# Kernel optimization log

Measured on AMD Instinct MI355X. Metric: run time of the kernel, lower is better.

Reference implementation:

```python
import jax, jax.numpy as jnp
import numpy as np

B, C_IN, H, W = 8, 32, 64, 64
C = 64  # num_channels


def setup_inputs() -> dict:
    key = jax.random.key(0)
    ks = jax.random.split(key, 9)
    s_in = 1.0 / np.sqrt(C_IN)
    s_c = 1.0 / np.sqrt(C)
    return {
        "x": jax.random.normal(ks[0], (B, C_IN, H, W), dtype=jnp.float32),
        "wq": jax.random.uniform(ks[1], (C, C_IN), jnp.float32, -s_in, s_in),
        "bq": jax.random.uniform(ks[2], (C,), jnp.float32, -s_in, s_in),
        "wk": jax.random.uniform(ks[3], (C, C_IN), jnp.float32, -s_in, s_in),
        "bk": jax.random.uniform(ks[4], (C,), jnp.float32, -s_in, s_in),
        "wv": jax.random.uniform(ks[5], (C, C_IN), jnp.float32, -s_in, s_in),
        "bv": jax.random.uniform(ks[6], (C,), jnp.float32, -s_in, s_in),
        "wo": jax.random.uniform(ks[7], (C_IN, C), jnp.float32, -s_c, s_c),
        "bo": jax.random.uniform(ks[8], (C_IN,), jnp.float32, -s_c, s_c),
    }


def reference(x, wq, bq, wk, bk, wv, bv, wo, bo):
    b, c_in, h, w = x.shape
    n = h * w
    # 1x1 convs == per-pixel linear projections; produce (B, N, C) directly
    q = (jnp.einsum('bchw,oc->bhwo', x, wq) + bq).reshape(b, n, -1)
    k = (jnp.einsum('bchw,oc->bhwo', x, wk) + bk).reshape(b, n, -1)
    v = (jnp.einsum('bchw,oc->bhwo', x, wv) + bv).reshape(b, n, -1)
    # unscaled attention over spatial positions (no 1/sqrt(d) in original)
    scores = jnp.einsum('bnc,bmc->bnm', q, k)  # (B, N, N)
    attn = jax.nn.softmax(scores, axis=-1)
    out = jnp.einsum('bnm,bmc->bnc', attn, v)  # (B, N, C)
    out = out.reshape(b, h, w, -1)
    out = jnp.einsum('bhwc,oc->bohw', out, wo) + bo[None, :, None, None]
    return out + x
```

## Files before the change

kernel.cpp:

```cpp
#include <hip/hip_runtime.h>
#include <hip/hip_bf16.h>

#define CIN    32
#define NPIX   4096
#define DIM    64
#define LOG2E  1.4426950408889634f

#if __has_builtin(__builtin_amdgcn_exp2f)
#define EXP2(x) __builtin_amdgcn_exp2f(x)
#else
#define EXP2(x) exp2f(x)
#endif

typedef float  f32x4  __attribute__((ext_vector_type(4)));
typedef float  f32x16 __attribute__((ext_vector_type(16)));
typedef short  s16x8  __attribute__((ext_vector_type(8)));

#define ZERO16 {0.f,0.f,0.f,0.f,0.f,0.f,0.f,0.f,0.f,0.f,0.f,0.f,0.f,0.f,0.f,0.f}

__device__ __forceinline__ f32x16 mfma32(s16x8 a, s16x8 b, f32x16 c) {
    return __builtin_amdgcn_mfma_f32_32x32x16_bf16(a, b, c, 0, 0, 0);
}


__global__ __launch_bounds__(256) void qkv_proj(
    const float* __restrict__ x,
    const float* __restrict__ wq, const float* __restrict__ bq,
    const float* __restrict__ wk, const float* __restrict__ bk,
    const float* __restrict__ wv, const float* __restrict__ bv,
    __hip_bfloat16* __restrict__ qb, __hip_bfloat16* __restrict__ kb,
    __hip_bfloat16* __restrict__ vb)
{
    const int tid  = threadIdx.x;
    const int wid  = tid >> 6;
    const int lane = tid & 63;
    const int l31  = lane & 31;
    const int hl   = lane >> 5;
    const int b    = blockIdx.y;
    const int bx   = blockIdx.x;
    const int s    = bx * 4 + wid;
    const int px   = s * 32 + l31;

    s16x8 xhi[2], xlo[2];
    #pragma unroll
    for (int kt = 0; kt < 2; kt++) {
        union { s16x8 v; __hip_bfloat16 h8[8]; } uh, ul;
        #pragma unroll
        for (int j = 0; j < 8; j++) {
            const int c = kt * 16 + hl * 8 + j;
            const float xv = x[((size_t)b * CIN + c) * NPIX + px];
            const __hip_bfloat16 hi = __float2bfloat16(xv);
            uh.h8[j] = hi;
            ul.h8[j] = __float2bfloat16(xv - __bfloat162float(hi));
        }
        xhi[kt] = uh.v; xlo[kt] = ul.v;
    }

    auto do_mat = [&](const float* __restrict__ W, const float* __restrict__ B,
                      int which) {
        const float scale = (which == 0) ? LOG2E : 1.0f;
        s16x8 whi[2][2], wlo[2][2];
        #pragma unroll
        for (int t = 0; t < 2; t++)
            #pragma unroll
            for (int kt = 0; kt < 2; kt++) {
                const float* wp = W + (size_t)(t * 32 + l31) * CIN + kt * 16 + hl * 8;
                f32x4 a0 = *(const f32x4*)wp;
                f32x4 a1 = *(const f32x4*)(wp + 4);
                union { s16x8 v; __hip_bfloat16 h8[8]; } uh, ul;
                #pragma unroll
                for (int j = 0; j < 4; j++) {
                    const float v0 = a0[j] * scale, v1 = a1[j] * scale;
                    const __hip_bfloat16 h0 = __float2bfloat16(v0);
                    const __hip_bfloat16 h1 = __float2bfloat16(v1);
                    uh.h8[j] = h0; uh.h8[4 + j] = h1;
                    ul.h8[j]     = __float2bfloat16(v0 - __bfloat162float(h0));
                    ul.h8[4 + j] = __float2bfloat16(v1 - __bfloat162float(h1));
                }
                whi[t][kt] = uh.v; wlo[t][kt] = ul.v;
            }

        f32x16 acc0 = ZERO16, acc1 = ZERO16;
        if (which < 2) {
            #pragma unroll
            for (int kt = 0; kt < 2; kt++) {
                acc0 = mfma32(whi[0][kt], xhi[kt], acc0);
                acc1 = mfma32(whi[1][kt], xhi[kt], acc1);
                acc0 = mfma32(whi[0][kt], xlo[kt], acc0);
                acc1 = mfma32(whi[1][kt], xlo[kt], acc1);
                acc0 = mfma32(wlo[0][kt], xhi[kt], acc0);
                acc1 = mfma32(wlo[1][kt], xhi[kt], acc1);
            }
            #pragma unroll
            for (int t = 0; t < 2; t++) {
                const f32x16 acc = t ? acc1 : acc0;
                #pragma unroll
                for (int ig = 0; ig < 4; ig++) {
                    f32x4 b4 = *(const f32x4*)(B + t * 32 + ig * 8 + hl * 4);
                    union { unsigned long long u; __hip_bfloat16 h4[4]; } st;
                    #pragma unroll
                    for (int r = 0; r < 4; r++)
                        st.h4[r] = __float2bfloat16(acc[ig * 4 + r] + b4[r] * scale);
                    if (which == 0) {
                        const size_t off = ((size_t)b * NPIX + px) * DIM
                                         + t * 32 + ig * 8 + hl * 4;
                        *(unsigned long long*)(qb + off) = st.u;
                    } else {
                        const size_t off = (size_t)b * 262144
                            + ((size_t)(s * 4 + 2 * t + (ig >> 1)) * 64
                               + (ig & 1) * 32 + l31) * 8 + 4 * hl;
                        *(unsigned long long*)(kb + off) = st.u;
                    }
                }
            }
        } else {
            #pragma unroll
            for (int kt = 0; kt < 2; kt++) {
                acc0 = mfma32(xhi[kt], whi[0][kt], acc0);
                acc1 = mfma32(xhi[kt], whi[1][kt], acc1);
                acc0 = mfma32(xlo[kt], whi[0][kt], acc0);
                acc1 = mfma32(xlo[kt], whi[1][kt], acc1);
                acc0 = mfma32(xhi[kt], wlo[0][kt], acc0);
                acc1 = mfma32(xhi[kt], wlo[1][kt], acc1);
            }
            #pragma unroll
            for (int t = 0; t < 2; t++) {
                const f32x16 acc = t ? acc1 : acc0;
                const float bvv = B[t * 32 + l31];
                #pragma unroll
                for (int m = 0; m < 2; m++) {
                    union { s16x8 v; __hip_bfloat16 h8[8]; } st;
                    #pragma unroll
                    for (int e = 0; e < 8; e++)
                        st.h8[e] = __float2bfloat16(acc[m * 8 + e] + bvv);
                    const size_t off = (size_t)b * 262144
                        + ((size_t)(s * 4 + 2 * t + m) * 64 + hl * 32 + l31) * 8;
                    *(s16x8*)(vb + off) = st.v;
                }
            }
        }
    };

    do_mat(wq, bq, 0);
    do_mat(wk, bk, 1);
    do_mat(wv, bv, 2);
}

__global__ __launch_bounds__(512, 2) void attn_fused(
    const __hip_bfloat16* __restrict__ qb,
    const __hip_bfloat16* __restrict__ kbf,
    const __hip_bfloat16* __restrict__ vbf,
    const float* __restrict__ wo, const float* __restrict__ bo,
    const float* __restrict__ x, float* __restrict__ y)
{
    __shared__ __align__(16) char  sm[2][8][4096];
    __shared__ __align__(16) float REDx[4][64][33];
    __shared__ float LRED2[4][32];

    const int tid  = threadIdx.x;
    const int w    = tid >> 6;
    const int g    = w >> 1;
    const int h    = w & 1;
    const int lane = tid & 63;
    const int q    = lane & 31;
    const int hl   = lane >> 5;
    const int b    = blockIdx.x;
    const int row0 = blockIdx.y * 128 + g * 32;

    s16x8 qf[4];
    #pragma unroll
    for (int kt = 0; kt < 4; kt++)
        qf[kt] = *(const s16x8*)(qb + ((size_t)b * NPIX + row0 + q) * DIM
                                 + kt * 16 + hl * 8);

    f32x16 o0 = ZERO16, o1 = ZERO16;
    float lsacc = 0.f;

    const char* stbase = ((w >> 2) ? (const char*)vbf : (const char*)kbf)
                       + (size_t)b * 524288
                       + (size_t)((w >> 1) & 1) * 262144
                       + (size_t)(w & 1) * 4096
                       + (size_t)lane * 16;
    char* std0 = &sm[0][w][lane * 16];
    char* std1 = &sm[1][w][lane * 16];

    #pragma unroll
    for (int i = 0; i < 4; i++)
        *(f32x4*)(std0 + i * 1024) = *(const f32x4*)(stbase + i * 1024);
    __syncthreads();

    int cur = 0;
    for (int p = 0; p < 32; ++p) {
        const size_t srcoff = (size_t)((p < 31) ? p + 1 : 31) * 8192;
        f32x4 r0 = *(const f32x4*)(stbase + srcoff);
        f32x4 r1 = *(const f32x4*)(stbase + srcoff + 1024);
        f32x4 r2 = *(const f32x4*)(stbase + srcoff + 2048);
        f32x4 r3 = *(const f32x4*)(stbase + srcoff + 3072);

        const char* K0 = sm[cur][h * 2 + 0];
        const char* K1 = sm[cur][h * 2 + 1];
        const char* V0 = sm[cur][4 + h * 2 + 0];
        const char* V1 = sm[cur][4 + h * 2 + 1];
        s16x8 kf0[4], kf1[4], vv0[4], vv1[4];
        #pragma unroll
        for (int i = 0; i < 4; i++) {
            kf0[i] = *(const s16x8*)(K0 + i * 1024 + lane * 16);
            kf1[i] = *(const s16x8*)(K1 + i * 1024 + lane * 16);
            vv0[i] = *(const s16x8*)(V0 + i * 1024 + lane * 16);
            vv1[i] = *(const s16x8*)(V1 + i * 1024 + lane * 16);
        }

        __builtin_amdgcn_s_setprio(1);
        f32x16 s0 = ZERO16, s1 = ZERO16;
        s0 = mfma32(kf0[0], qf[0], s0);
        s1 = mfma32(kf1[0], qf[0], s1);
        s0 = mfma32(kf0[1], qf[1], s0);
        s1 = mfma32(kf1[1], qf[1], s1);
        s0 = mfma32(kf0[2], qf[2], s0);
        s1 = mfma32(kf1[2], qf[2], s1);
        s0 = mfma32(kf0[3], qf[3], s0);
        s1 = mfma32(kf1[3], qf[3], s1);
        __builtin_amdgcn_s_setprio(0);

        union { s16x8 v; __hip_bfloat16 h8[8]; } p00, p01, p10, p11;
        #pragma unroll
        for (int r = 0; r < 16; r++) { s0[r] = EXP2(s0[r]); lsacc += s0[r]; }
        #pragma unroll
        for (int j = 0; j < 8; j++) {
            p00.h8[j] = __float2bfloat16(s0[j]);
            p01.h8[j] = __float2bfloat16(s0[8 + j]);
        }
        #pragma unroll
        for (int r = 0; r < 16; r++) { s1[r] = EXP2(s1[r]); lsacc += s1[r]; }
        #pragma unroll
        for (int j = 0; j < 8; j++) {
            p10.h8[j] = __float2bfloat16(s1[j]);
            p11.h8[j] = __float2bfloat16(s1[8 + j]);
        }

        __builtin_amdgcn_s_setprio(1);
        o0 = mfma32(vv0[0], p00.v, o0);
        o1 = mfma32(vv0[2], p00.v, o1);
        o0 = mfma32(vv0[1], p01.v, o0);
        o1 = mfma32(vv0[3], p01.v, o1);
        o0 = mfma32(vv1[0], p10.v, o0);
        o1 = mfma32(vv1[2], p10.v, o1);
        o0 = mfma32(vv1[1], p11.v, o0);
        o1 = mfma32(vv1[3], p11.v, o1);
        __builtin_amdgcn_s_setprio(0);

        char* dst = cur ? std0 : std1;
        *(f32x4*)(dst)        = r0;
        *(f32x4*)(dst + 1024) = r1;
        *(f32x4*)(dst + 2048) = r2;
        *(f32x4*)(dst + 3072) = r3;
        __syncthreads();
        cur ^= 1;
    }

    lsacc += __shfl_xor(lsacc, 32, 64);

    if (h == 1) {
        #pragma unroll
        for (int i = 0; i < 16; i++) {
            const int rr = (i & 3) + 8 * (i >> 2) + 4 * hl;
            REDx[g][rr][q]      = o0[i];
            REDx[g][32 + rr][q] = o1[i];
        }
        if (hl == 0) LRED2[g][q] = lsacc;
    }
    __syncthreads();

    if (h == 0) {
        const float lsum = lsacc + LRED2[g][q];
        #pragma unroll
        for (int i = 0; i < 16; i++) {
            const int rr = (i & 3) + 8 * (i >> 2) + 4 * hl;
            o0[i] += REDx[g][rr][q];
            o1[i] += REDx[g][32 + rr][q];
        }
        const float inv = 1.0f / lsum;

        s16x8 pbo[4];
        #pragma unroll
        for (int gg = 0; gg < 4; gg++) {
            union { s16x8 v; __hip_bfloat16 h8[8]; } pk;
            #pragma unroll
            for (int j = 0; j < 8; j++) {
                const float vv2 = (gg < 2) ? o0[(gg & 1) * 8 + j] : o1[(gg & 1) * 8 + j];
                pk.h8[j] = __float2bfloat16(vv2 * inv);
            }
            pbo[gg] = pk.v;
        }

        s16x8 aw[4];
        #pragma unroll
        for (int gg = 0; gg < 4; gg++) {
            f32x4 w0 = *(const f32x4*)(wo + (size_t)q * DIM + gg * 16 + hl * 4);
            f32x4 w1 = *(const f32x4*)(wo + (size_t)q * DIM + gg * 16 + 8 + hl * 4);
            union { s16x8 v; __hip_bfloat16 h8[8]; } wf;
            #pragma unroll
            for (int j = 0; j < 4; j++) {
                wf.h8[j]     = __float2bfloat16(w0[j]);
                wf.h8[4 + j] = __float2bfloat16(w1[j]);
            }
            aw[gg] = wf.v;
        }

        f32x16 d = ZERO16;
        #pragma unroll
        for (int gg = 0; gg < 4; gg++)
            d = mfma32(aw[gg], pbo[gg], d);

        #pragma unroll
        for (int i = 0; i < 16; i++) {
            const int out = (i & 3) + 8 * (i >> 2) + 4 * hl;
            const int row = row0 + q;
            const size_t xi = ((size_t)b * CIN + out) * NPIX + row;
            y[xi] = d[i] + bo[out] + x[xi];
        }
    }
}

extern "C" void kernel_launch(void* const* d_in, const int* in_sizes, int n_in,
                              void* d_out, int out_size, void* d_ws, size_t ws_size,
                              hipStream_t stream)
{
    const float* x  = (const float*)d_in[0];
    const float* wq = (const float*)d_in[1];
    const float* bq = (const float*)d_in[2];
    const float* wk = (const float*)d_in[3];
    const float* bk = (const float*)d_in[4];
    const float* wv = (const float*)d_in[5];
    const float* bv = (const float*)d_in[6];
    const float* wo = (const float*)d_in[7];
    const float* bo = (const float*)d_in[8];
    float* y = (float*)d_out;

    char* ws = (char*)d_ws;
    __hip_bfloat16* qb = (__hip_bfloat16*)(ws);
    __hip_bfloat16* kb = (__hip_bfloat16*)(ws + (4u << 20));
    __hip_bfloat16* vb = (__hip_bfloat16*)(ws + (8u << 20));

    qkv_proj<<<dim3(32, 8), dim3(256), 0, stream>>>(x, wq, bq, wk, bk, wv, bv, qb, kb, vb);
    attn_fused<<<dim3(8, 32), dim3(512), 0, stream>>>(qb, kb, vb, wo, bo, x, y);
}
```

Before: 118.2 us.

## Repartition attention waves so each wave handles two query tiles over one key quarter

Each wave now owns 64 query rows (two 32-row tiles) and one quarter of the key range, instead of 32 rows and half the keys. Each K/V fragment read from shared memory is reused across two query tiles, which halves LDS fragment reads per MFMA. The final cross-wave reduction becomes a two-stage tree through the staging buffer, which removes the separate REDx array and shrinks shared memory. In exchange it needs more accumulator registers and adds extra barriers in the epilogue.

After: 117.1 us. About the same (-1.0%).

```diff
diff --git a/kernel.cpp b/kernel.cpp
--- a/kernel.cpp
+++ b/kernel.cpp
@@ -153,33 +153,38 @@
     const float* __restrict__ wo, const float* __restrict__ bo,
     const float* __restrict__ x, float* __restrict__ y)
 {
-    __shared__ __align__(16) char  sm[2][8][4096];
-    __shared__ __align__(16) float REDx[4][64][33];
-    __shared__ float LRED2[4][32];
+    __shared__ __align__(16) char sm[2][8][4096];
+    __shared__ float LRA[2][2][2][32];
+    __shared__ float LRB[2][2][32];
+
+    float* REDp = (float*)&sm[0][0][0];
 
     const int tid  = threadIdx.x;
     const int w    = tid >> 6;
-    const int g    = w >> 1;
-    const int h    = w & 1;
+    const int qh   = w >> 2;
+    const int kq   = w & 3;
     const int lane = tid & 63;
     const int q    = lane & 31;
     const int hl   = lane >> 5;
     const int b    = blockIdx.x;
-    const int row0 = blockIdx.y * 128 + g * 32;
-
-    s16x8 qf[4];
+    const int row0 = blockIdx.y * 128 + qh * 64;
+
+    s16x8 qfA[4], qfB[4];
     #pragma unroll
-    for (int kt = 0; kt < 4; kt++)
-        qf[kt] = *(const s16x8*)(qb + ((size_t)b * NPIX + row0 + q) * DIM
-                                 + kt * 16 + hl * 8);
-
-    f32x16 o0 = ZERO16, o1 = ZERO16;
-    float lsacc = 0.f;
+    for (int kt = 0; kt < 4; kt++) {
+        qfA[kt] = *(const s16x8*)(qb + ((size_t)b * NPIX + row0 + q) * DIM
+                                  + kt * 16 + hl * 8);
+        qfB[kt] = *(const s16x8*)(qb + ((size_t)b * NPIX + row0 + 32 + q) * DIM
+                                  + kt * 16 + hl * 8);
+    }
+
+    f32x16 oA0 = ZERO16, oA1 = ZERO16;
+    f32x16 oB0 = ZERO16, oB1 = ZERO16;
+    float lsA = 0.f, lsB = 0.f;
 
     const char* stbase = ((w >> 2) ? (const char*)vbf : (const char*)kbf)
                        + (size_t)b * 524288
-                       + (size_t)((w >> 1) & 1) * 262144
-                       + (size_t)(w & 1) * 4096
+                       + (size_t)(w & 3) * 131072
                        + (size_t)lane * 16;
     char* std0 = &sm[0][w][lane * 16];
     char* std1 = &sm[1][w][lane * 16];
@@ -191,62 +196,58 @@
 
     int cur = 0;
     for (int p = 0; p < 32; ++p) {
-        const size_t srcoff = (size_t)((p < 31) ? p + 1 : 31) * 8192;
+        const size_t srcoff = (size_t)((p < 31) ? p + 1 : 31) * 4096;
         f32x4 r0 = *(const f32x4*)(stbase + srcoff);
         f32x4 r1 = *(const f32x4*)(stbase + srcoff + 1024);
         f32x4 r2 = *(const f32x4*)(stbase + srcoff + 2048);
         f32x4 r3 = *(const f32x4*)(stbase + srcoff + 3072);
 
-        const char* K0 = sm[cur][h * 2 + 0];
-        const char* K1 = sm[cur][h * 2 + 1];
-        const char* V0 = sm[cur][4 + h * 2 + 0];
-        const char* V1 = sm[cur][4 + h * 2 + 1];
-        s16x8 kf0[4], kf1[4], vv0[4], vv1[4];
+        const char* Kl = sm[cur][kq];
+        const char* Vl = sm[cur][4 + kq];
+        s16x8 kf[4], vv[4];
         #pragma unroll
         for (int i = 0; i < 4; i++) {
-            kf0[i] = *(const s16x8*)(K0 + i * 1024 + lane * 16);
-            kf1[i] = *(const s16x8*)(K1 + i * 1024 + lane * 16);
-            vv0[i] = *(const s16x8*)(V0 + i * 1024 + lane * 16);
-            vv1[i] = *(const s16x8*)(V1 + i * 1024 + lane * 16);
+            kf[i] = *(const s16x8*)(Kl + i * 1024 + lane * 16);
+            vv[i] = *(const s16x8*)(Vl + i * 1024 + lane * 16);
         }
 
         __builtin_amdgcn_s_setprio(1);
-        f32x16 s0 = ZERO16, s1 = ZERO16;
-        s0 = mfma32(kf0[0], qf[0], s0);
-        s1 = mfma32(kf1[0], qf[0], s1);
-        s0 = mfma32(kf0[1], qf[1], s0);
-        s1 = mfma32(kf1[1], qf[1], s1);
-        s0 = mfma32(kf0[2], qf[2], s0);
-        s1 = mfma32(kf1[2], qf[2], s1);
-        s0 = mfma32(kf0[3], qf[3], s0);
-        s1 = mfma32(kf1[3], qf[3], s1);
+        f32x16 sA = ZERO16, sB = ZERO16;
+        sA = mfma32(kf[0], qfA[0], sA);
+        sB = mfma32(kf[0], qfB[0], sB);
+        sA = mfma32(kf[1], qfA[1], sA);
+        sB = mfma32(kf[1], qfB[1], sB);
+        sA = mfma32(kf[2], qfA[2], sA);
+        sB = mfma32(kf[2], qfB[2], sB);
+        sA = mfma32(kf[3], qfA[3], sA);
+        sB = mfma32(kf[3], qfB[3], sB);
         __builtin_amdgcn_s_setprio(0);
 
-        union { s16x8 v; __hip_bfloat16 h8[8]; } p00, p01, p10, p11;
-        #pragma unroll
-        for (int r = 0; r < 16; r++) { s0[r] = EXP2(s0[r]); lsacc += s0[r]; }
+        union { s16x8 v; __hip_bfloat16 h8[8]; } pA0, pA1, pB0, pB1;
+        #pragma unroll
+        for (int r = 0; r < 16; r++) { sA[r] = EXP2(sA[r]); lsA += sA[r]; }
         #pragma unroll
         for (int j = 0; j < 8; j++) {
-            p00.h8[j] = __float2bfloat16(s0[j]);
-            p01.h8[j] = __float2bfloat16(s0[8 + j]);
-        }
-        #pragma unroll
-        for (int r = 0; r < 16; r++) { s1[r] = EXP2(s1[r]); lsacc += s1[r]; }
+            pA0.h8[j] = __float2bfloat16(sA[j]);
+            pA1.h8[j] = __float2bfloat16(sA[8 + j]);
+        }
+        #pragma unroll
+        for (int r = 0; r < 16; r++) { sB[r] = EXP2(sB[r]); lsB += sB[r]; }
         #pragma unroll
         for (int j = 0; j < 8; j++) {
-            p10.h8[j] = __float2bfloat16(s1[j]);
-            p11.h8[j] = __float2bfloat16(s1[8 + j]);
+            pB0.h8[j] = __float2bfloat16(sB[j]);
+            pB1.h8[j] = __float2bfloat16(sB[8 + j]);
         }
 
         __builtin_amdgcn_s_setprio(1);
-        o0 = mfma32(vv0[0], p00.v, o0);
-        o1 = mfma32(vv0[2], p00.v, o1);
-        o0 = mfma32(vv0[1], p01.v, o0);
-        o1 = mfma32(vv0[3], p01.v, o1);
-        o0 = mfma32(vv1[0], p10.v, o0);
-        o1 = mfma32(vv1[2], p10.v, o1);
-        o0 = mfma32(vv1[1], p11.v, o0);
-        o1 = mfma32(vv1[3], p11.v, o1);
+        oA0 = mfma32(vv[0], pA0.v, oA0);
+        oA1 = mfma32(vv[2], pA0.v, oA1);
+        oB0 = mfma32(vv[0], pB0.v, oB0);
+        oB1 = mfma32(vv[2], pB0.v, oB1);
+        oA0 = mfma32(vv[1], pA1.v, oA0);
+        oA1 = mfma32(vv[3], pA1.v, oA1);
+        oB0 = mfma32(vv[1], pB1.v, oB0);
+        oB1 = mfma32(vv[3], pB1.v, oB1);
         __builtin_amdgcn_s_setprio(0);
 
         char* dst = cur ? std0 : std1;
@@ -258,40 +259,74 @@
         cur ^= 1;
     }
 
-    lsacc += __shfl_xor(lsacc, 32, 64);
-
-    if (h == 1) {
-        #pragma unroll
-        for (int i = 0; i < 16; i++) {
-            const int rr = (i & 3) + 8 * (i >> 2) + 4 * hl;
-            REDx[g][rr][q]      = o0[i];
-            REDx[g][32 + rr][q] = o1[i];
-        }
-        if (hl == 0) LRED2[g][q] = lsacc;
+    lsA += __shfl_xor(lsA, 32, 64);
+    lsB += __shfl_xor(lsB, 32, 64);
+
+    if (kq >= 2) {
+        #pragma unroll
+        for (int t = 0; t < 2; t++) {
+            float* S = REDp + (size_t)((kq - 2) * 4 + qh * 2 + t) * 2048;
+            const f32x16& p0 = t ? oB0 : oA0;
+            const f32x16& p1 = t ? oB1 : oA1;
+            #pragma unroll
+            for (int i = 0; i < 16; i++) {
+                const int rr = (i & 3) + 8 * (i >> 2) + 4 * hl;
+                S[rr * 32 + q]        = p0[i];
+                S[(32 + rr) * 32 + q] = p1[i];
+            }
+            if (hl == 0) LRA[kq - 2][qh][t][q] = t ? lsB : lsA;
+        }
     }
     __syncthreads();
-
-    if (h == 0) {
-        const float lsum = lsacc + LRED2[g][q];
-        #pragma unroll
-        for (int i = 0; i < 16; i++) {
-            const int rr = (i & 3) + 8 * (i >> 2) + 4 * hl;
-            o0[i] += REDx[g][rr][q];
-            o1[i] += REDx[g][32 + rr][q];
-        }
-        const float inv = 1.0f / lsum;
-
-        s16x8 pbo[4];
-        #pragma unroll
-        for (int gg = 0; gg < 4; gg++) {
-            union { s16x8 v; __hip_bfloat16 h8[8]; } pk;
-            #pragma unroll
-            for (int j = 0; j < 8; j++) {
-                const float vv2 = (gg < 2) ? o0[(gg & 1) * 8 + j] : o1[(gg & 1) * 8 + j];
-                pk.h8[j] = __float2bfloat16(vv2 * inv);
-            }
-            pbo[gg] = pk.v;
-        }
+    if (kq < 2) {
+        #pragma unroll
+        for (int t = 0; t < 2; t++) {
+            const float* S = REDp + (size_t)(kq * 4 + qh * 2 + t) * 2048;
+            f32x16& p0 = t ? oB0 : oA0;
+            f32x16& p1 = t ? oB1 : oA1;
+            #pragma unroll
+            for (int i = 0; i < 16; i++) {
+                const int rr = (i & 3) + 8 * (i >> 2) + 4 * hl;
+                p0[i] += S[rr * 32 + q];
+                p1[i] += S[(32 + rr) * 32 + q];
+            }
+        }
+        lsA += LRA[kq][qh][0][q];
+        lsB += LRA[kq][qh][1][q];
+    }
+    __syncthreads();
+    if (kq == 1) {
+        #pragma unroll
+        for (int t = 0; t < 2; t++) {
+            float* S = REDp + (size_t)(qh * 2 + t) * 2048;
+            const f32x16& p0 = t ? oB0 : oA0;
+            const f32x16& p1 = t ? oB1 : oA1;
+            #pragma unroll
+            for (int i = 0; i < 16; i++) {
+                const int rr = (i & 3) + 8 * (i >> 2) + 4 * hl;
+                S[rr * 32 + q]        = p0[i];
+                S[(32 + rr) * 32 + q] = p1[i];
+            }
+            if (hl == 0) LRB[qh][t][q] = t ? lsB : lsA;
+        }
+    }
+    __syncthreads();
+
+    if (kq == 0) {
+        #pragma unroll
+        for (int t = 0; t < 2; t++) {
+            const float* S = REDp + (size_t)(qh * 2 + t) * 2048;
+            f32x16& p0 = t ? oB0 : oA0;
+            f32x16& p1 = t ? oB1 : oA1;
+            #pragma unroll
+            for (int i = 0; i < 16; i++) {
+                const int rr = (i & 3) + 8 * (i >> 2) + 4 * hl;
+                p0[i] += S[rr * 32 + q];
+                p1[i] += S[(32 + rr) * 32 + q];
+            }
+        }
+        lsA += LRB[qh][0][q];
+        lsB += LRB[qh][1][q];
 
         s16x8 aw[4];
         #pragma unroll
@@ -307,17 +342,37 @@
             aw[gg] = wf.v;
         }
 
-        f32x16 d = ZERO16;
-        #pragma unroll
-        for (int gg = 0; gg < 4; gg++)
-            d = mfma32(aw[gg], pbo[gg], d);
-
-        #pragma unroll
-        for (int i = 0; i < 16; i++) {
-            const int out = (i & 3) + 8 * (i >> 2) + 4 * hl;
-            const int row = row0 + q;
-            const size_t xi = ((size_t)b * CIN + out) * NPIX + row;
-            y[xi] = d[i] + bo[out] + x[xi];
+        #pragma unroll
+        for (int t = 0; t < 2; t++) {
+            const f32x16& p0 = t ? oB0 : oA0;
+            const f32x16& p1 = t ? oB1 : oA1;
+            const float inv = 1.0f / (t ? lsB : lsA);
+
+            s16x8 pbo[4];
+            #pragma unroll
+            for (int gg = 0; gg < 4; gg++) {
+                union { s16x8 v; __hip_bfloat16 h8[8]; } pk;
+                #pragma unroll
+                for (int j = 0; j < 8; j++) {
+                    const float vv2 = (gg < 2) ? p0[(gg & 1) * 8 + j]
+                                               : p1[(gg & 1) * 8 + j];
+                    pk.h8[j] = __float2bfloat16(vv2 * inv);
+                }
+                pbo[gg] = pk.v;
+            }
+
+            f32x16 d = ZERO16;
+            #pragma unroll
+            for (int gg = 0; gg < 4; gg++)
+                d = mfma32(aw[gg], pbo[gg], d);
+
+            #pragma unroll
+            for (int i = 0; i < 16; i++) {
+                const int out = (i & 3) + 8 * (i >> 2) + 4 * hl;
+                const int row = row0 + t * 32 + q;
+                const size_t xi = ((size_t)b * CIN + out) * NPIX + row;
+                y[xi] = d[i] + bo[out] + x[xi];
+            }
         }
     }
 }
```

## Split keys four ways per query group and double the attention grid

Applied to the files above, without the earlier changes.

Each attention block now covers 64 query rows with two groups of four waves, and each wave handles a quarter of the key/value tiles. The grid doubles to 512 blocks. The cross-wave reduction buffer now aliases the staging LDS, which shrinks shared memory so launch bounds can request 4 blocks per CU. The aim is more occupancy and parallelism; the cost is re-streaming K/V from global for twice as many blocks, plus a larger final reduction. The setprio hints are also dropped.

Result: slower. 123.7 us (+4.6%).

```diff
diff --git a/kernel.cpp b/kernel.cpp
--- a/kernel.cpp
+++ b/kernel.cpp
@@ -146,26 +146,27 @@
     do_mat(wv, bv, 2);
 }
 
-__global__ __launch_bounds__(512, 2) void attn_fused(
+__global__ __launch_bounds__(512, 4) void attn_fused(
     const __hip_bfloat16* __restrict__ qb,
     const __hip_bfloat16* __restrict__ kbf,
     const __hip_bfloat16* __restrict__ vbf,
     const float* __restrict__ wo, const float* __restrict__ bo,
     const float* __restrict__ x, float* __restrict__ y)
 {
-    __shared__ __align__(16) char  sm[2][8][4096];
-    __shared__ __align__(16) float REDx[4][64][33];
-    __shared__ float LRED2[4][32];
+    __shared__ __align__(16) char sm[2][8][4096];
+    __shared__ float LRED2[3][2][32];
+
+    float (*REDq)[2][64][33] = (float (*)[2][64][33])&sm[0][0][0];
 
     const int tid  = threadIdx.x;
     const int w    = tid >> 6;
-    const int g    = w >> 1;
-    const int h    = w & 1;
+    const int g    = w >> 2;
+    const int kq   = w & 3;
     const int lane = tid & 63;
     const int q    = lane & 31;
     const int hl   = lane >> 5;
     const int b    = blockIdx.x;
-    const int row0 = blockIdx.y * 128 + g * 32;
+    const int row0 = blockIdx.y * 64 + g * 32;
 
     s16x8 qf[4];
     #pragma unroll
@@ -178,8 +179,7 @@
 
     const char* stbase = ((w >> 2) ? (const char*)vbf : (const char*)kbf)
                        + (size_t)b * 524288
-                       + (size_t)((w >> 1) & 1) * 262144
-                       + (size_t)(w & 1) * 4096
+                       + (size_t)(w & 3) * 131072
                        + (size_t)lane * 16;
     char* std0 = &sm[0][w][lane * 16];
     char* std1 = &sm[1][w][lane * 16];
@@ -191,63 +191,44 @@
 
     int cur = 0;
     for (int p = 0; p < 32; ++p) {
-        const size_t srcoff = (size_t)((p < 31) ? p + 1 : 31) * 8192;
+        const char* Kl = sm[cur][kq];
+        s16x8 kf[4];
+        #pragma unroll
+        for (int i = 0; i < 4; i++)
+            kf[i] = *(const s16x8*)(Kl + i * 1024 + lane * 16);
+
+        const size_t srcoff = (size_t)((p < 31) ? p + 1 : 31) * 4096;
         f32x4 r0 = *(const f32x4*)(stbase + srcoff);
         f32x4 r1 = *(const f32x4*)(stbase + srcoff + 1024);
         f32x4 r2 = *(const f32x4*)(stbase + srcoff + 2048);
         f32x4 r3 = *(const f32x4*)(stbase + srcoff + 3072);
 
-        const char* K0 = sm[cur][h * 2 + 0];
-        const char* K1 = sm[cur][h * 2 + 1];
-        const char* V0 = sm[cur][4 + h * 2 + 0];
-        const char* V1 = sm[cur][4 + h * 2 + 1];
-        s16x8 kf0[4], kf1[4], vv0[4], vv1[4];
-        #pragma unroll
-        for (int i = 0; i < 4; i++) {
-            kf0[i] = *(const s16x8*)(K0 + i * 1024 + lane * 16);
-            kf1[i] = *(const s16x8*)(K1 + i * 1024 + lane * 16);
-            vv0[i] = *(const s16x8*)(V0 + i * 1024 + lane * 16);
-            vv1[i] = *(const s16x8*)(V1 + i * 1024 + lane * 16);
-        }
-
-        __builtin_amdgcn_s_setprio(1);
-        f32x16 s0 = ZERO16, s1 = ZERO16;
-        s0 = mfma32(kf0[0], qf[0], s0);
-        s1 = mfma32(kf1[0], qf[0], s1);
-        s0 = mfma32(kf0[1], qf[1], s0);
-        s1 = mfma32(kf1[1], qf[1], s1);
-        s0 = mfma32(kf0[2], qf[2], s0);
-        s1 = mfma32(kf1[2], qf[2], s1);
-        s0 = mfma32(kf0[3], qf[3], s0);
-        s1 = mfma32(kf1[3], qf[3], s1);
-        __builtin_amdgcn_s_setprio(0);
-
-        union { s16x8 v; __hip_bfloat16 h8[8]; } p00, p01, p10, p11;
-        #pragma unroll
-        for (int r = 0; r < 16; r++) { s0[r] = EXP2(s0[r]); lsacc += s0[r]; }
+        f32x16 s = ZERO16;
+        s = mfma32(kf[0], qf[0], s);
+        s = mfma32(kf[1], qf[1], s);
+        s = mfma32(kf[2], qf[2], s);
+        s = mfma32(kf[3], qf[3], s);
+
+        union { s16x8 v; __hip_bfloat16 h8[8]; } p0, p1;
         #pragma unroll
         for (int j = 0; j < 8; j++) {
-            p00.h8[j] = __float2bfloat16(s0[j]);
-            p01.h8[j] = __float2bfloat16(s0[8 + j]);
-        }
-        #pragma unroll
-        for (int r = 0; r < 16; r++) { s1[r] = EXP2(s1[r]); lsacc += s1[r]; }
-        #pragma unroll
-        for (int j = 0; j < 8; j++) {
-            p10.h8[j] = __float2bfloat16(s1[j]);
-            p11.h8[j] = __float2bfloat16(s1[8 + j]);
-        }
-
-        __builtin_amdgcn_s_setprio(1);
-        o0 = mfma32(vv0[0], p00.v, o0);
-        o1 = mfma32(vv0[2], p00.v, o1);
-        o0 = mfma32(vv0[1], p01.v, o0);
-        o1 = mfma32(vv0[3], p01.v, o1);
-        o0 = mfma32(vv1[0], p10.v, o0);
-        o1 = mfma32(vv1[2], p10.v, o1);
-        o0 = mfma32(vv1[1], p11.v, o0);
-        o1 = mfma32(vv1[3], p11.v, o1);
-        __builtin_amdgcn_s_setprio(0);
+            float e0 = EXP2(s[j]);
+            float e1 = EXP2(s[8 + j]);
+            lsacc += e0 + e1;
+            p0.h8[j] = __float2bfloat16(e0);
+            p1.h8[j] = __float2bfloat16(e1);
+        }
+
+        const char* Vl = sm[cur][4 + kq];
+        s16x8 vv[4];
+        #pragma unroll
+        for (int i = 0; i < 4; i++)
+            vv[i] = *(const s16x8*)(Vl + i * 1024 + lane * 16);
+
+        o0 = mfma32(vv[0], p0.v, o0);
+        o1 = mfma32(vv[2], p0.v, o1);
+        o0 = mfma32(vv[1], p1.v, o0);
+        o1 = mfma32(vv[3], p1.v, o1);
 
         char* dst = cur ? std0 : std1;
         *(f32x4*)(dst)        = r0;
@@ -260,26 +241,29 @@
 
     lsacc += __shfl_xor(lsacc, 32, 64);
 
-    if (h == 1) {
+    if (kq != 0) {
         #pragma unroll
         for (int i = 0; i < 16; i++) {
             const int rr = (i & 3) + 8 * (i >> 2) + 4 * hl;
-            REDx[g][rr][q]      = o0[i];
-            REDx[g][32 + rr][q] = o1[i];
-        }
-        if (hl == 0) LRED2[g][q] = lsacc;
+            REDq[kq - 1][g][rr][q]      = o0[i];
+            REDq[kq - 1][g][32 + rr][q] = o1[i];
+        }
+        if (hl == 0) LRED2[kq - 1][g][q] = lsacc;
     }
     __syncthreads();
 
-    if (h == 0) {
-        const float lsum = lsacc + LRED2[g][q];
-        #pragma unroll
-        for (int i = 0; i < 16; i++) {
-            const int rr = (i & 3) + 8 * (i >> 2) + 4 * hl;
-            o0[i] += REDx[g][rr][q];
-            o1[i] += REDx[g][32 + rr][q];
-        }
-        const float inv = 1.0f / lsum;
+    if (kq == 0) {
+        #pragma unroll
+        for (int sl = 0; sl < 3; sl++) {
+            lsacc += LRED2[sl][g][q];
+            #pragma unroll
+            for (int i = 0; i < 16; i++) {
+                const int rr = (i & 3) + 8 * (i >> 2) + 4 * hl;
+                o0[i] += REDq[sl][g][rr][q];
+                o1[i] += REDq[sl][g][32 + rr][q];
+            }
+        }
+        const float inv = 1.0f / lsacc;
 
         s16x8 pbo[4];
         #pragma unroll
@@ -343,5 +327,5 @@
     __hip_bfloat16* vb = (__hip_bfloat16*)(ws + (8u << 20));
 
     qkv_proj<<<dim3(32, 8), dim3(256), 0, stream>>>(x, wq, bq, wk, bk, wv, bv, qb, kb, vb);
-    attn_fused<<<dim3(8, 32), dim3(512), 0, stream>>>(qb, kb, vb, wo, bo, x, y);
+    attn_fused<<<dim3(8, 64), dim3(512), 0, stream>>>(qb, kb, vb, wo, bo, x, y);
 }
```
